# Kernel tuning notes

Hardware: AMD Instinct MI355X
Metric: run time of the kernel (lower is better)

Reference implementation:

```python
import jax, jax.numpy as jnp
import numpy as np
from jax import lax

B, L = 8, 2048
TOP_K = 30
NUM_RBF = 16
NUM_POS = 16
NODE_IN, EDGE_IN = 6, NUM_POS + NUM_RBF  # features_type='dist'
H = 128  # node_features == edge_features


def setup_inputs() -> dict:
    key = jax.random.key(0)
    ks = jax.random.split(key, 4)
    # coords scaled so pairwise distances span the RBF range [0, 20]
    X = jax.random.normal(ks[0], (B, L, 4, 3), dtype=jnp.float32) * 10.0
    mask = jnp.ones((B, L), dtype=jnp.float32)
    W_node = jax.random.normal(ks[1], (NODE_IN, H), dtype=jnp.float32) * 0.1
    b_node = jnp.zeros((H,), dtype=jnp.float32)
    W_edge = jax.random.normal(ks[2], (EDGE_IN, H), dtype=jnp.float32) * 0.1
    b_edge = jnp.zeros((H,), dtype=jnp.float32)
    gamma_n = jnp.ones((H,), dtype=jnp.float32)
    beta_n = jnp.zeros((H,), dtype=jnp.float32)
    gamma_e = jnp.ones((H,), dtype=jnp.float32)
    beta_e = jnp.zeros((H,), dtype=jnp.float32)
    return {"X": X, "mask": mask, "W_node": W_node, "b_node": b_node,
            "W_edge": W_edge, "b_edge": b_edge, "gamma_n": gamma_n,
            "beta_n": beta_n, "gamma_e": gamma_e, "beta_e": beta_e}


def _dist(X_ca, mask, eps=1e-6):
    # masked pairwise Euclidean distances + kNN (smallest)
    mask_2D = mask[:, None, :] * mask[:, :, None]            # [B,L,L]
    dX = X_ca[:, None, :, :] - X_ca[:, :, None, :]           # [B,L,L,3]
    D = mask_2D * jnp.sqrt(jnp.sum(dX * dX, axis=-1) + eps)  # [B,L,L]
    D_max = jnp.max(D, axis=-1, keepdims=True)
    D_adjust = D + (1.0 - mask_2D) * (D_max + 1.0)
    neg_D, E_idx = lax.top_k(-D_adjust, TOP_K)               # smallest-k
    return -neg_D, E_idx                                     # [B,L,K], [B,L,K]


def _rbf(D):
    D_mu = jnp.linspace(0.0, 20.0, NUM_RBF)                  # [R]
    D_sigma = 20.0 / NUM_RBF
    return jnp.exp(-(((D[..., None] - D_mu) / D_sigma) ** 2))  # [B,L,K,R]


def _positional_encodings(E_idx):
    # directional differential positional encodings
    N_nodes = E_idx.shape[1]
    ii = jnp.arange(N_nodes, dtype=jnp.float32)[None, :, None]
    d = (E_idx.astype(jnp.float32) - ii)[..., None]          # [B,L,K,1]
    freq = jnp.exp(jnp.arange(0, NUM_POS, 2, dtype=jnp.float32)
                   * (-(np.log(10000.0) / NUM_POS)))          # [P/2]
    angles = d * freq                                        # [B,L,K,P/2]
    return jnp.concatenate([jnp.cos(angles), jnp.sin(angles)], axis=-1)


def _dihedrals(X, eps=1e-7):
    # phi/psi/omega from N,CA,C backbone trace -> [B,L,6]
    b, n = X.shape[0], X.shape[1]
    Xb = X[:, :, :3, :].reshape(b, 3 * n, 3)
    dX = Xb[:, 1:, :] - Xb[:, :-1, :]
    U = dX / (jnp.linalg.norm(dX, axis=-1, keepdims=True) + 1e-8)
    u_2, u_1, u_0 = U[:, :-2], U[:, 1:-1], U[:, 2:]
    n_2 = jnp.cross(u_2, u_1)
    n_2 = n_2 / (jnp.linalg.norm(n_2, axis=-1, keepdims=True) + 1e-8)
    n_1 = jnp.cross(u_1, u_0)
    n_1 = n_1 / (jnp.linalg.norm(n_1, axis=-1, keepdims=True) + 1e-8)
    cosD = jnp.clip(jnp.sum(n_2 * n_1, axis=-1), -1.0 + eps, 1.0 - eps)
    Dang = jnp.sign(jnp.sum(u_2 * n_1, axis=-1)) * jnp.arccos(cosD)
    Dang = jnp.pad(Dang, ((0, 0), (1, 2)))
    Dang = Dang.reshape(b, n, 3)
    return jnp.concatenate([jnp.cos(Dang), jnp.sin(Dang)], axis=-1)


def _layer_norm(x, gamma, beta, eps=1e-5):
    mu = jnp.mean(x, axis=-1, keepdims=True)
    var = jnp.mean((x - mu) ** 2, axis=-1, keepdims=True)
    return (x - mu) * lax.rsqrt(var + eps) * gamma + beta


def reference(X, mask, W_node, b_node, W_edge, b_edge,
              gamma_n, beta_n, gamma_e, beta_e):
    X_ca = X[:, :, 1, :]
    D_neighbors, E_idx = _dist(X_ca, mask)
    E_positional = _positional_encodings(E_idx)              # [B,L,K,P]
    RBF = _rbf(D_neighbors)                                  # [B,L,K,R]
    V = _dihedrals(X)                                        # [B,L,6]
    E = jnp.concatenate([E_positional, RBF], axis=-1)        # [B,L,K,P+R]
    V = _layer_norm(V @ W_node + b_node, gamma_n, beta_n)
    E = _layer_norm(E @ W_edge + b_edge, gamma_e, beta_e)
    return V, E, E_idx
```

## Files before the change

### kernel.cpp

```cpp
#include <hip/hip_runtime.h>
#include <cstdint>
#include <cstddef>

#define NB 8
#define NL 2048
#define TOPK 30
#define NH 128
#define CAND_CAP 256

typedef unsigned long long ull;
typedef __attribute__((ext_vector_type(8))) short short8v;
typedef __attribute__((ext_vector_type(4))) float f32x4;

__device__ __forceinline__ short f2bf(float f) {
    unsigned int b = __float_as_uint(f);
    b += 0x7fffu + ((b >> 16) & 1u);
    return (short)(b >> 16);
}

__global__ __launch_bounds__(256) void vnx_kernel(
    const float* __restrict__ X, const float* __restrict__ mask,
    const float* __restrict__ Wn, const float* __restrict__ bn,
    const float* __restrict__ gn, const float* __restrict__ btn,
    float* __restrict__ V, float4* __restrict__ P)
{
    __shared__ float fsh[64][8];

    const int tid = threadIdx.x;
    const int node_base = blockIdx.x * 64;

    if (tid < 64) {
        const int ln   = tid;
        const int node = node_base + ln;
        const int b = node >> 11, i = node & (NL - 1);

        const int h0 = ln, h1 = ln + 64;
        float w0[6], w1[6];
        #pragma unroll
        for (int j = 0; j < 6; ++j) { w0[j] = Wn[j * NH + h0]; w1[j] = Wn[j * NH + h1]; }
        const float bb0 = bn[h0], bb1 = bn[h1];

        float st[35];
        {
            int idx = 0;
            #pragma unroll
            for (int j = 0; j < 6; ++j)
                #pragma unroll
                for (int k = j; k < 6; ++k)
                    st[idx++] = w0[j] * w0[k] + w1[j] * w1[k];
            #pragma unroll
            for (int j = 0; j < 6; ++j) st[21 + j] = w0[j] * bb0 + w1[j] * bb1;
            #pragma unroll
            for (int j = 0; j < 6; ++j) st[27 + j] = w0[j] + w1[j];
            st[33] = bb0 + bb1;
            st[34] = bb0 * bb0 + bb1 * bb1;
            #pragma unroll
            for (int q = 0; q < 35; ++q) {
                float vv = st[q];
                #pragma unroll
                for (int off = 32; off; off >>= 1) vv += __shfl_xor(vv, off);
                st[q] = vv;
            }
        }

        const float* XB = X + (size_t)b * NL * 12;
        const int rm1 = (i >= 1) ? i - 1 : 0;
        const int rp1 = (i <= NL - 2) ? i + 1 : NL - 1;
        float p[6][3];
        {
            const int rows[6]  = { rm1, i, i, i, rp1, rp1 };
            const int atoms[6] = { 2,   0, 1, 2, 0,   1   };
            #pragma unroll
            for (int k = 0; k < 6; ++k) {
                const float* q = XB + ((size_t)rows[k] * 4 + atoms[k]) * 3;
                p[k][0] = q[0]; p[k][1] = q[1]; p[k][2] = q[2];
            }
        }
        P[node] = make_float4(p[2][0], p[2][1], p[2][2], mask[node]);

        float uv[5][3], nv[4][3];
        #pragma unroll
        for (int k = 0; k < 5; ++k) {
            float vx = p[k+1][0] - p[k][0];
            float vy = p[k+1][1] - p[k][1];
            float vz = p[k+1][2] - p[k][2];
            float n = sqrtf(vx*vx + vy*vy + vz*vz) + 1e-8f;
            uv[k][0] = vx / n; uv[k][1] = vy / n; uv[k][2] = vz / n;
        }
        #pragma unroll
        for (int k = 0; k < 4; ++k) {
            float cx = uv[k][1]*uv[k+1][2] - uv[k][2]*uv[k+1][1];
            float cy = uv[k][2]*uv[k+1][0] - uv[k][0]*uv[k+1][2];
            float cz = uv[k][0]*uv[k+1][1] - uv[k][1]*uv[k+1][0];
            float n = sqrtf(cx*cx + cy*cy + cz*cz) + 1e-8f;
            nv[k][0] = cx / n; nv[k][1] = cy / n; nv[k][2] = cz / n;
        }
        float f[6];
        #pragma unroll
        for (int a = 0; a < 3; ++a) {
            bool valid = (a == 0) ? (i >= 1) : (i <= NL - 2);
            float cosD = nv[a][0]*nv[a+1][0] + nv[a][1]*nv[a+1][1] + nv[a][2]*nv[a+1][2];
            cosD = fminf(fmaxf(cosD, -1.0f + 1e-7f), 1.0f - 1e-7f);
            float sg = uv[a][0]*nv[a+1][0] + uv[a][1]*nv[a+1][1] + uv[a][2]*nv[a+1][2];
            float sgn = (sg > 0.0f) ? 1.0f : ((sg < 0.0f) ? -1.0f : 0.0f);
            float an = valid ? (sgn * acosf(cosD)) : 0.0f;
            f[a]     = cosf(an);
            f[3 + a] = sinf(an);
        }

        float s1 = st[33];
        #pragma unroll
        for (int j = 0; j < 6; ++j) s1 = fmaf(f[j], st[27 + j], s1);
        float qd = st[34];
        #pragma unroll
        for (int j = 0; j < 6; ++j) qd = fmaf(2.0f * f[j], st[21 + j], qd);
        {
            int idx = 0;
            #pragma unroll
            for (int j = 0; j < 6; ++j)
                #pragma unroll
                for (int k = j; k < 6; ++k) {
                    float coef = (j == k) ? 1.0f : 2.0f;
                    qd = fmaf(coef * f[j] * f[k], st[idx], qd);
                    ++idx;
                }
        }
        const float mean = s1 * (1.0f / 128.0f);
        const float var  = fmaxf(qd * (1.0f / 128.0f) - mean * mean, 0.0f);
        const float inv  = rsqrtf(var + 1e-5f);

        #pragma unroll
        for (int j = 0; j < 6; ++j) fsh[ln][j] = f[j];
        fsh[ln][6] = mean;
        fsh[ln][7] = inv;
    }
    __syncthreads();

    const int m  = tid & 31;
    const int ng = tid >> 5;
    const int h4 = m * 4;
    f32x4 w4[6];
    #pragma unroll
    for (int j = 0; j < 6; ++j) w4[j] = *(const f32x4*)&Wn[j * NH + h4];
    const f32x4 b4  = *(const f32x4*)&bn [h4];
    const f32x4 g4  = *(const f32x4*)&gn [h4];
    const f32x4 bt4 = *(const f32x4*)&btn[h4];

    #pragma unroll
    for (int it = 0; it < 8; ++it) {
        const int nn = it * 8 + ng;
        const float* fr = fsh[nn];
        f32x4 a = b4;
        #pragma unroll
        for (int j = 0; j < 6; ++j) {
            const float fj = fr[j];
            #pragma unroll
            for (int x = 0; x < 4; ++x) a[x] = fmaf(fj, w4[j][x], a[x]);
        }
        const float mn = fr[6], iv = fr[7];
        f32x4 o;
        #pragma unroll
        for (int x = 0; x < 4; ++x) o[x] = (a[x] - mn) * iv * g4[x] + bt4[x];
        *(f32x4*)&V[(size_t)(node_base + nn) * NH + h4] = o;
    }
}

__global__ __launch_bounds__(256) void topk_kernel(
    const float4* __restrict__ P,
    float* __restrict__ eidx, float* __restrict__ dnb)
{
    __shared__ float4 Ps[NL];
    __shared__ ull cand[4][CAND_CAP];

    const int tid = threadIdx.x;
    const int wv  = tid >> 6;
    const int ln  = tid & 63;
    const int row = blockIdx.x * 4 + wv;
    const int b   = row >> 11;
    const int i   = row & (NL - 1);

    const float4* Pb = P + (size_t)b * NL;
    #pragma unroll
    for (int q = 0; q < 8; ++q) Ps[tid + 256 * q] = Pb[tid + 256 * q];
    __syncthreads();

    const float4 pi = Ps[i];
    const float xi = pi.x, yi = pi.y, zi = pi.z, mi = pi.w;

    unsigned int u[32];
    float lm0 = 0.0f, lm1 = 0.0f, lm2 = 0.0f, lm3 = 0.0f;
    #pragma unroll
    for (int t = 0; t < 32; t += 4) {
        #pragma unroll
        for (int q = 0; q < 4; ++q) {
            const float4 pj = Ps[ln + 64 * (t + q)];
            float dx = xi - pj.x;
            float dy = yi - pj.y;
            float dz = zi - pj.z;
            float s = __fadd_rn(__fmul_rn(dx, dx), __fmul_rn(dy, dy));
            s = __fadd_rn(s, __fmul_rn(dz, dz));
            s = __fadd_rn(s, 1e-6f);
            float m2 = __fmul_rn(pj.w, mi);
            float d  = __fmul_rn(m2, __fsqrt_rn(s));
            u[t + q] = __float_as_uint(d) | ((m2 == 0.0f) ? 0x80000000u : 0u);
            if      (q == 0) lm0 = fmaxf(lm0, d);
            else if (q == 1) lm1 = fmaxf(lm1, d);
            else if (q == 2) lm2 = fmaxf(lm2, d);
            else             lm3 = fmaxf(lm3, d);
        }
    }
    float lmax = fmaxf(fmaxf(lm0, lm1), fmaxf(lm2, lm3));
    #pragma unroll
    for (int off = 32; off; off >>= 1) lmax = fmaxf(lmax, __shfl_xor(lmax, off));
    const unsigned int DMB = __float_as_uint(__fadd_rn(lmax, 1.0f));

    unsigned int um0 = 0xFFFFFFFFu, um1 = 0xFFFFFFFFu,
                 um2 = 0xFFFFFFFFu, um3 = 0xFFFFFFFFu;
    #pragma unroll
    for (int t = 0; t < 32; t += 4) {
        unsigned int b0 = (u[t+0] & 0x80000000u) ? DMB : u[t+0];
        unsigned int b1 = (u[t+1] & 0x80000000u) ? DMB : u[t+1];
        unsigned int b2 = (u[t+2] & 0x80000000u) ? DMB : u[t+2];
        unsigned int b3 = (u[t+3] & 0x80000000u) ? DMB : u[t+3];
        u[t+0] = b0; u[t+1] = b1; u[t+2] = b2; u[t+3] = b3;
        um0 = min(um0, b0); um1 = min(um1, b1);
        um2 = min(um2, b2); um3 = min(um3, b3);
    }
    unsigned int umin = min(min(um0, um1), min(um2, um3));

    unsigned int v = umin;
    #pragma unroll
    for (int k = 2; k <= 64; k <<= 1) {
        #pragma unroll
        for (int j = k >> 1; j > 0; j >>= 1) {
            unsigned int o = __shfl_xor(v, j);
            bool asc   = ((ln & k) == 0);
            bool lower = ((ln & j) == 0);
            v = (lower == asc) ? min(v, o) : max(v, o);
        }
    }
    const unsigned int T = __shfl(v, TOPK - 1);

    unsigned int base = 0;
    #pragma unroll
    for (int t = 0; t < 32; ++t) {
        bool act = u[t] <= T;
        ull m = __ballot(act);
        if (act) {
            unsigned int pos = base + (unsigned)__popcll(m & ((1ull << ln) - 1ull));
            if (pos < CAND_CAP)
                cand[wv][pos] = ((ull)u[t] << 32) | (unsigned)(ln + 64 * t);
        }
        base += (unsigned)__popcll(m);
    }
    const unsigned int cnt = base;

    float* eo  = eidx + (size_t)row * TOPK;
    float* dno = dnb  + (size_t)row * TOPK;

    if (cnt <= CAND_CAP) {
        ull k0 = ((unsigned)ln        < cnt) ? cand[wv][ln]        : ~0ULL;
        ull k1 = ((unsigned)ln +  64u < cnt) ? cand[wv][ln +  64]  : ~0ULL;
        ull k2 = ((unsigned)ln + 128u < cnt) ? cand[wv][ln + 128]  : ~0ULL;
        ull k3 = ((unsigned)ln + 192u < cnt) ? cand[wv][ln + 192]  : ~0ULL;
        int r0 = 0, r1 = 0, r2 = 0, r3 = 0;
        for (unsigned int p = 0; p < cnt; p += 4) {
            ull c0 = cand[wv][p];
            ull c1 = (p + 1 < cnt) ? cand[wv][p + 1] : ~0ULL;
            ull c2 = (p + 2 < cnt) ? cand[wv][p + 2] : ~0ULL;
            ull c3 = (p + 3 < cnt) ? cand[wv][p + 3] : ~0ULL;
            r0 += (c0 < k0) + (c1 < k0) + (c2 < k0) + (c3 < k0);
            r1 += (c0 < k1) + (c1 < k1) + (c2 < k1) + (c3 < k1);
            r2 += (c0 < k2) + (c1 < k2) + (c2 < k2) + (c3 < k2);
            r3 += (c0 < k3) + (c1 < k3) + (c2 < k3) + (c3 < k3);
        }
        if (r0 < TOPK) { eo[r0] = (float)(unsigned)(k0 & 0xFFFFFFFFu); dno[r0] = __uint_as_float((unsigned)(k0 >> 32)); }
        if (r1 < TOPK) { eo[r1] = (float)(unsigned)(k1 & 0xFFFFFFFFu); dno[r1] = __uint_as_float((unsigned)(k1 >> 32)); }
        if (r2 < TOPK) { eo[r2] = (float)(unsigned)(k2 & 0xFFFFFFFFu); dno[r2] = __uint_as_float((unsigned)(k2 >> 32)); }
        if (r3 < TOPK) { eo[r3] = (float)(unsigned)(k3 & 0xFFFFFFFFu); dno[r3] = __uint_as_float((unsigned)(k3 >> 32)); }
    } else {
        ull last = 0ULL;
        for (int k = 0; k < TOPK; ++k) {
            ull best = ~0ULL;
            #pragma unroll
            for (int t = 0; t < 32; ++t) {
                ull key = ((ull)u[t] << 32) | (unsigned)(ln + 64 * t);
                if (key > last && key < best) best = key;
            }
            #pragma unroll
            for (int off = 32; off; off >>= 1) {
                ull o = __shfl_xor(best, off);
                if (o < best) best = o;
            }
            if (ln == 0) {
                eo[k]  = (float)(unsigned)(best & 0xFFFFFFFFu);
                dno[k] = __uint_as_float((unsigned)(best >> 32));
            }
            last = best;
        }
    }
}

__global__ __launch_bounds__(256) void edge_kernel(
    const float* __restrict__ eidx, const float* __restrict__ dnb,
    const float* __restrict__ We, const float* __restrict__ be,
    const float* __restrict__ ge, const float* __restrict__ bte,
    float* __restrict__ E)
{
    __shared__ float ebuf[4][16][132];
    const int lane = threadIdx.x & 63;
    const int wv   = threadIdx.x >> 6;
    const int c    = lane & 15;
    const int g    = lane >> 4;
    const int wid  = (int)((blockIdx.x * blockDim.x + threadIdx.x) >> 6);
    const int nw   = (int)((gridDim.x * blockDim.x) >> 6);

    short8v W[8];
    #pragma unroll
    for (int t = 0; t < 8; ++t)
        #pragma unroll
        for (int e = 0; e < 8; ++e)
            W[t][e] = f2bf(We[(g * 8 + e) * NH + t * 16 + c]);

    float fcs[8];
    #pragma unroll
    for (int e = 0; e < 8; ++e) {
        if (g < 2) fcs[e] = expf((float)(2 * e) * -0.57564627f);
        else       fcs[e] = (float)((g - 2) * 8 + e) * (20.0f / 15.0f);
    }

    const int ntiles = NB * NL * TOPK / 16;
    for (int tile = wid; tile < ntiles; tile += nw) {
        const int e0   = tile * 16;
        const int edge = e0 + c;
        const float fidx = eidx[edge];
        const float Dv   = dnb[edge];
        const int   row  = edge / TOPK;
        const float d    = fidx - (float)(row & (NL - 1));

        short8v F;
        if (g == 0) {
            #pragma unroll
            for (int e = 0; e < 8; ++e) F[e] = f2bf(cosf(d * fcs[e]));
        } else if (g == 1) {
            #pragma unroll
            for (int e = 0; e < 8; ++e) F[e] = f2bf(sinf(d * fcs[e]));
        } else {
            #pragma unroll
            for (int e = 0; e < 8; ++e) {
                float tt = (Dv - fcs[e]) * 0.8f;
                F[e] = f2bf(expf(-tt * tt));
            }
        }

        f32x4 acc[8];
        const f32x4 zero = {0.0f, 0.0f, 0.0f, 0.0f};
        #pragma unroll
        for (int t = 0; t < 8; ++t)
            acc[t] = __builtin_amdgcn_mfma_f32_16x16x32_bf16(W[t], F, zero, 0, 0, 0);

        float s = 0.0f, s2 = 0.0f;
        #pragma unroll
        for (int t = 0; t < 8; ++t) {
            const f32x4 b4 = *(const f32x4*)&be[t * 16 + g * 4];
            #pragma unroll
            for (int j = 0; j < 4; ++j) {
                float vv = acc[t][j] + b4[j];
                acc[t][j] = vv;
                s  += vv;
                s2 = fmaf(vv, vv, s2);
            }
        }
        s  += __shfl_xor(s, 16);  s  += __shfl_xor(s, 32);
        s2 += __shfl_xor(s2, 16); s2 += __shfl_xor(s2, 32);
        const float mean = s * (1.0f / 128.0f);
        const float var  = fmaxf(s2 * (1.0f / 128.0f) - mean * mean, 0.0f);
        const float inv  = rsqrtf(var + 1e-5f);

        #pragma unroll
        for (int t = 0; t < 8; ++t) {
            const f32x4 g4  = *(const f32x4*)&ge [t * 16 + g * 4];
            const f32x4 bt4 = *(const f32x4*)&bte[t * 16 + g * 4];
            f32x4 o;
            #pragma unroll
            for (int j = 0; j < 4; ++j)
                o[j] = (acc[t][j] - mean) * inv * g4[j] + bt4[j];
            *(f32x4*)&ebuf[wv][c][t * 16 + g * 4] = o;
        }

        float* const Ebase = E + (size_t)e0 * NH;
        #pragma unroll
        for (int q = 0; q < 8; ++q) {
            const int fi = q * 256 + lane * 4;
            const int ce = fi >> 7;
            const int id = fi & 127;
            const f32x4 o = *(const f32x4*)&ebuf[wv][ce][id];
            __builtin_nontemporal_store(o, (f32x4*)&Ebase[(size_t)ce * NH + id]);
        }
    }
}

extern "C" void kernel_launch(void* const* d_in, const int* in_sizes, int n_in,
                              void* d_out, int out_size, void* d_ws, size_t ws_size,
                              hipStream_t stream)
{
    const float* X    = (const float*)d_in[0];
    const float* mask = (const float*)d_in[1];
    const float* Wn   = (const float*)d_in[2];
    const float* bn   = (const float*)d_in[3];
    const float* We   = (const float*)d_in[4];
    const float* be   = (const float*)d_in[5];
    const float* gn   = (const float*)d_in[6];
    const float* btn  = (const float*)d_in[7];
    const float* ge   = (const float*)d_in[8];
    const float* bte  = (const float*)d_in[9];

    float* out = (float*)d_out;
    float* V   = out;
    float* E   = V  + (size_t)NB * NL * NH;
    float* EI  = E  + (size_t)NB * NL * TOPK * NH;

    float4* P  = (float4*)d_ws;
    float* dnb = (float*)d_ws + 4 * (size_t)NB * NL;

    hipLaunchKernelGGL(vnx_kernel,  dim3(NB * NL / 64),  dim3(256), 0, stream,
                       X, mask, Wn, bn, gn, btn, V, P);
    hipLaunchKernelGGL(topk_kernel, dim3(NB * NL / 4),   dim3(256), 0, stream,
                       P, EI, dnb);
    hipLaunchKernelGGL(edge_kernel, dim3(1920),          dim3(256), 0, stream,
                       EI, dnb, We, be, ge, bte, E);
}
```

Measured before the change: 120.4 us.

## Merge node-feature kernel into edge kernel and load CA coords directly in topk

```diff
diff --git a/kernel.cpp b/kernel.cpp
--- a/kernel.cpp
+++ b/kernel.cpp
@@ -7,6 +7,8 @@
 #define TOPK 30
 #define NH 128
 #define CAND_CAP 256
+#define EDGE_BLOCKS 1920
+#define EDGE_WAVES (EDGE_BLOCKS * 4)
 
 typedef unsigned long long ull;
 typedef __attribute__((ext_vector_type(8))) short short8v;
@@ -18,170 +20,28 @@
     return (short)(b >> 16);
 }
 
-__global__ __launch_bounds__(256) void vnx_kernel(
+__global__ __launch_bounds__(512) void topk_kernel(
     const float* __restrict__ X, const float* __restrict__ mask,
-    const float* __restrict__ Wn, const float* __restrict__ bn,
-    const float* __restrict__ gn, const float* __restrict__ btn,
-    float* __restrict__ V, float4* __restrict__ P)
-{
-    __shared__ float fsh[64][8];
-
-    const int tid = threadIdx.x;
-    const int node_base = blockIdx.x * 64;
-
-    if (tid < 64) {
-        const int ln   = tid;
-        const int node = node_base + ln;
-        const int b = node >> 11, i = node & (NL - 1);
-
-        const int h0 = ln, h1 = ln + 64;
-        float w0[6], w1[6];
-        #pragma unroll
-        for (int j = 0; j < 6; ++j) { w0[j] = Wn[j * NH + h0]; w1[j] = Wn[j * NH + h1]; }
-        const float bb0 = bn[h0], bb1 = bn[h1];
-
-        float st[35];
-        {
-            int idx = 0;
-            #pragma unroll
-            for (int j = 0; j < 6; ++j)
-                #pragma unroll
-                for (int k = j; k < 6; ++k)
-                    st[idx++] = w0[j] * w0[k] + w1[j] * w1[k];
-            #pragma unroll
-            for (int j = 0; j < 6; ++j) st[21 + j] = w0[j] * bb0 + w1[j] * bb1;
-            #pragma unroll
-            for (int j = 0; j < 6; ++j) st[27 + j] = w0[j] + w1[j];
-            st[33] = bb0 + bb1;
-            st[34] = bb0 * bb0 + bb1 * bb1;
-            #pragma unroll
-            for (int q = 0; q < 35; ++q) {
-                float vv = st[q];
-                #pragma unroll
-                for (int off = 32; off; off >>= 1) vv += __shfl_xor(vv, off);
-                st[q] = vv;
-            }
-        }
-
-        const float* XB = X + (size_t)b * NL * 12;
-        const int rm1 = (i >= 1) ? i - 1 : 0;
-        const int rp1 = (i <= NL - 2) ? i + 1 : NL - 1;
-        float p[6][3];
-        {
-            const int rows[6]  = { rm1, i, i, i, rp1, rp1 };
-            const int atoms[6] = { 2,   0, 1, 2, 0,   1   };
-            #pragma unroll
-            for (int k = 0; k < 6; ++k) {
-                const float* q = XB + ((size_t)rows[k] * 4 + atoms[k]) * 3;
-                p[k][0] = q[0]; p[k][1] = q[1]; p[k][2] = q[2];
-            }
-        }
-        P[node] = make_float4(p[2][0], p[2][1], p[2][2], mask[node]);
-
-        float uv[5][3], nv[4][3];
-        #pragma unroll
-        for (int k = 0; k < 5; ++k) {
-            float vx = p[k+1][0] - p[k][0];
-            float vy = p[k+1][1] - p[k][1];
-            float vz = p[k+1][2] - p[k][2];
-            float n = sqrtf(vx*vx + vy*vy + vz*vz) + 1e-8f;
-            uv[k][0] = vx / n; uv[k][1] = vy / n; uv[k][2] = vz / n;
-        }
-        #pragma unroll
-        for (int k = 0; k < 4; ++k) {
-            float cx = uv[k][1]*uv[k+1][2] - uv[k][2]*uv[k+1][1];
-            float cy = uv[k][2]*uv[k+1][0] - uv[k][0]*uv[k+1][2];
-            float cz = uv[k][0]*uv[k+1][1] - uv[k][1]*uv[k+1][0];
-            float n = sqrtf(cx*cx + cy*cy + cz*cz) + 1e-8f;
-            nv[k][0] = cx / n; nv[k][1] = cy / n; nv[k][2] = cz / n;
-        }
-        float f[6];
-        #pragma unroll
-        for (int a = 0; a < 3; ++a) {
-            bool valid = (a == 0) ? (i >= 1) : (i <= NL - 2);
-            float cosD = nv[a][0]*nv[a+1][0] + nv[a][1]*nv[a+1][1] + nv[a][2]*nv[a+1][2];
-            cosD = fminf(fmaxf(cosD, -1.0f + 1e-7f), 1.0f - 1e-7f);
-            float sg = uv[a][0]*nv[a+1][0] + uv[a][1]*nv[a+1][1] + uv[a][2]*nv[a+1][2];
-            float sgn = (sg > 0.0f) ? 1.0f : ((sg < 0.0f) ? -1.0f : 0.0f);
-            float an = valid ? (sgn * acosf(cosD)) : 0.0f;
-            f[a]     = cosf(an);
-            f[3 + a] = sinf(an);
-        }
-
-        float s1 = st[33];
-        #pragma unroll
-        for (int j = 0; j < 6; ++j) s1 = fmaf(f[j], st[27 + j], s1);
-        float qd = st[34];
-        #pragma unroll
-        for (int j = 0; j < 6; ++j) qd = fmaf(2.0f * f[j], st[21 + j], qd);
-        {
-            int idx = 0;
-            #pragma unroll
-            for (int j = 0; j < 6; ++j)
-                #pragma unroll
-                for (int k = j; k < 6; ++k) {
-                    float coef = (j == k) ? 1.0f : 2.0f;
-                    qd = fmaf(coef * f[j] * f[k], st[idx], qd);
-                    ++idx;
-                }
-        }
-        const float mean = s1 * (1.0f / 128.0f);
-        const float var  = fmaxf(qd * (1.0f / 128.0f) - mean * mean, 0.0f);
-        const float inv  = rsqrtf(var + 1e-5f);
-
-        #pragma unroll
-        for (int j = 0; j < 6; ++j) fsh[ln][j] = f[j];
-        fsh[ln][6] = mean;
-        fsh[ln][7] = inv;
-    }
-    __syncthreads();
-
-    const int m  = tid & 31;
-    const int ng = tid >> 5;
-    const int h4 = m * 4;
-    f32x4 w4[6];
-    #pragma unroll
-    for (int j = 0; j < 6; ++j) w4[j] = *(const f32x4*)&Wn[j * NH + h4];
-    const f32x4 b4  = *(const f32x4*)&bn [h4];
-    const f32x4 g4  = *(const f32x4*)&gn [h4];
-    const f32x4 bt4 = *(const f32x4*)&btn[h4];
-
-    #pragma unroll
-    for (int it = 0; it < 8; ++it) {
-        const int nn = it * 8 + ng;
-        const float* fr = fsh[nn];
-        f32x4 a = b4;
-        #pragma unroll
-        for (int j = 0; j < 6; ++j) {
-            const float fj = fr[j];
-            #pragma unroll
-            for (int x = 0; x < 4; ++x) a[x] = fmaf(fj, w4[j][x], a[x]);
-        }
-        const float mn = fr[6], iv = fr[7];
-        f32x4 o;
-        #pragma unroll
-        for (int x = 0; x < 4; ++x) o[x] = (a[x] - mn) * iv * g4[x] + bt4[x];
-        *(f32x4*)&V[(size_t)(node_base + nn) * NH + h4] = o;
-    }
-}
-
-__global__ __launch_bounds__(256) void topk_kernel(
-    const float4* __restrict__ P,
     float* __restrict__ eidx, float* __restrict__ dnb)
 {
     __shared__ float4 Ps[NL];
-    __shared__ ull cand[4][CAND_CAP];
+    __shared__ ull cand[8][CAND_CAP];
 
     const int tid = threadIdx.x;
     const int wv  = tid >> 6;
     const int ln  = tid & 63;
-    const int row = blockIdx.x * 4 + wv;
+    const int row = blockIdx.x * 8 + wv;
     const int b   = row >> 11;
     const int i   = row & (NL - 1);
 
-    const float4* Pb = P + (size_t)b * NL;
-    #pragma unroll
-    for (int q = 0; q < 8; ++q) Ps[tid + 256 * q] = Pb[tid + 256 * q];
+    const float* Xb = X + (size_t)b * NL * 12;
+    const float* Mb = mask + (size_t)b * NL;
+    #pragma unroll
+    for (int q = 0; q < 4; ++q) {
+        const int j = tid + 512 * q;
+        const float* x = Xb + (size_t)j * 12 + 3;
+        Ps[j] = make_float4(x[0], x[1], x[2], Mb[j]);
+    }
     __syncthreads();
 
     const float4 pi = Ps[i];
@@ -301,102 +161,247 @@
     }
 }
 
-__global__ __launch_bounds__(256) void edge_kernel(
+__global__ __launch_bounds__(256) void edge_vn_kernel(
     const float* __restrict__ eidx, const float* __restrict__ dnb,
     const float* __restrict__ We, const float* __restrict__ be,
     const float* __restrict__ ge, const float* __restrict__ bte,
-    float* __restrict__ E)
+    float* __restrict__ E,
+    const float* __restrict__ X,  const float* __restrict__ Wn,
+    const float* __restrict__ bn, const float* __restrict__ gn,
+    const float* __restrict__ btn, float* __restrict__ V)
 {
-    __shared__ float ebuf[4][16][132];
-    const int lane = threadIdx.x & 63;
-    const int wv   = threadIdx.x >> 6;
-    const int c    = lane & 15;
-    const int g    = lane >> 4;
-    const int wid  = (int)((blockIdx.x * blockDim.x + threadIdx.x) >> 6);
-    const int nw   = (int)((gridDim.x * blockDim.x) >> 6);
-
-    short8v W[8];
-    #pragma unroll
-    for (int t = 0; t < 8; ++t)
-        #pragma unroll
-        for (int e = 0; e < 8; ++e)
-            W[t][e] = f2bf(We[(g * 8 + e) * NH + t * 16 + c]);
-
-    float fcs[8];
-    #pragma unroll
-    for (int e = 0; e < 8; ++e) {
-        if (g < 2) fcs[e] = expf((float)(2 * e) * -0.57564627f);
-        else       fcs[e] = (float)((g - 2) * 8 + e) * (20.0f / 15.0f);
-    }
-
-    const int ntiles = NB * NL * TOPK / 16;
-    for (int tile = wid; tile < ntiles; tile += nw) {
-        const int e0   = tile * 16;
-        const int edge = e0 + c;
-        const float fidx = eidx[edge];
-        const float Dv   = dnb[edge];
-        const int   row  = edge / TOPK;
-        const float d    = fidx - (float)(row & (NL - 1));
-
-        short8v F;
-        if (g == 0) {
-            #pragma unroll
-            for (int e = 0; e < 8; ++e) F[e] = f2bf(cosf(d * fcs[e]));
-        } else if (g == 1) {
-            #pragma unroll
-            for (int e = 0; e < 8; ++e) F[e] = f2bf(sinf(d * fcs[e]));
-        } else {
-            #pragma unroll
-            for (int e = 0; e < 8; ++e) {
-                float tt = (Dv - fcs[e]) * 0.8f;
-                F[e] = f2bf(expf(-tt * tt));
-            }
-        }
-
-        f32x4 acc[8];
-        const f32x4 zero = {0.0f, 0.0f, 0.0f, 0.0f};
+    __shared__ float shmem[4 * 16 * 132];
+
+    const int tid  = threadIdx.x;
+    const int lane = tid & 63;
+    const int wv   = tid >> 6;
+
+    if (blockIdx.x < EDGE_BLOCKS) {
+        float (*ebuf)[132] = (float(*)[132])(shmem + wv * 16 * 132);
+        const int c = lane & 15;
+        const int g = lane >> 4;
+        const int wid = blockIdx.x * 4 + wv;
+
+        short8v W[8];
         #pragma unroll
         for (int t = 0; t < 8; ++t)
-            acc[t] = __builtin_amdgcn_mfma_f32_16x16x32_bf16(W[t], F, zero, 0, 0, 0);
-
-        float s = 0.0f, s2 = 0.0f;
-        #pragma unroll
-        for (int t = 0; t < 8; ++t) {
-            const f32x4 b4 = *(const f32x4*)&be[t * 16 + g * 4];
-            #pragma unroll
-            for (int j = 0; j < 4; ++j) {
-                float vv = acc[t][j] + b4[j];
-                acc[t][j] = vv;
-                s  += vv;
-                s2 = fmaf(vv, vv, s2);
-            }
-        }
-        s  += __shfl_xor(s, 16);  s  += __shfl_xor(s, 32);
-        s2 += __shfl_xor(s2, 16); s2 += __shfl_xor(s2, 32);
-        const float mean = s * (1.0f / 128.0f);
-        const float var  = fmaxf(s2 * (1.0f / 128.0f) - mean * mean, 0.0f);
+            #pragma unroll
+            for (int e = 0; e < 8; ++e)
+                W[t][e] = f2bf(We[(g * 8 + e) * NH + t * 16 + c]);
+
+        float fcs[8];
+        #pragma unroll
+        for (int e = 0; e < 8; ++e) {
+            if (g < 2) fcs[e] = expf((float)(2 * e) * -0.57564627f);
+            else       fcs[e] = (float)((g - 2) * 8 + e) * (20.0f / 15.0f);
+        }
+
+        const int ntiles = NB * NL * TOPK / 16;
+        for (int tile = wid; tile < ntiles; tile += EDGE_WAVES) {
+            const int e0   = tile * 16;
+            const int edge = e0 + c;
+            const float fidx = eidx[edge];
+            const float Dv   = dnb[edge];
+            const int   row  = edge / TOPK;
+            const float d    = fidx - (float)(row & (NL - 1));
+
+            short8v F;
+            if (g == 0) {
+                #pragma unroll
+                for (int e = 0; e < 8; ++e) F[e] = f2bf(cosf(d * fcs[e]));
+            } else if (g == 1) {
+                #pragma unroll
+                for (int e = 0; e < 8; ++e) F[e] = f2bf(sinf(d * fcs[e]));
+            } else {
+                #pragma unroll
+                for (int e = 0; e < 8; ++e) {
+                    float tt = (Dv - fcs[e]) * 0.8f;
+                    F[e] = f2bf(expf(-tt * tt));
+                }
+            }
+
+            f32x4 acc[8];
+            const f32x4 zero = {0.0f, 0.0f, 0.0f, 0.0f};
+            #pragma unroll
+            for (int t = 0; t < 8; ++t)
+                acc[t] = __builtin_amdgcn_mfma_f32_16x16x32_bf16(W[t], F, zero, 0, 0, 0);
+
+            float s = 0.0f, s2 = 0.0f;
+            #pragma unroll
+            for (int t = 0; t < 8; ++t) {
+                const f32x4 b4 = *(const f32x4*)&be[t * 16 + g * 4];
+                #pragma unroll
+                for (int j = 0; j < 4; ++j) {
+                    float vv = acc[t][j] + b4[j];
+                    acc[t][j] = vv;
+                    s  += vv;
+                    s2 = fmaf(vv, vv, s2);
+                }
+            }
+            s  += __shfl_xor(s, 16);  s  += __shfl_xor(s, 32);
+            s2 += __shfl_xor(s2, 16); s2 += __shfl_xor(s2, 32);
+            const float mean = s * (1.0f / 128.0f);
+            const float var  = fmaxf(s2 * (1.0f / 128.0f) - mean * mean, 0.0f);
+            const float inv  = rsqrtf(var + 1e-5f);
+
+            #pragma unroll
+            for (int t = 0; t < 8; ++t) {
+                const f32x4 g4  = *(const f32x4*)&ge [t * 16 + g * 4];
+                const f32x4 bt4 = *(const f32x4*)&bte[t * 16 + g * 4];
+                f32x4 o;
+                #pragma unroll
+                for (int j = 0; j < 4; ++j)
+                    o[j] = (acc[t][j] - mean) * inv * g4[j] + bt4[j];
+                *(f32x4*)&ebuf[c][t * 16 + g * 4] = o;
+            }
+
+            float* const Ebase = E + (size_t)e0 * NH;
+            #pragma unroll
+            for (int q = 0; q < 8; ++q) {
+                const int fi = q * 256 + lane * 4;
+                const int ce = fi >> 7;
+                const int id = fi & 127;
+                const f32x4 o = *(const f32x4*)&ebuf[ce][id];
+                __builtin_nontemporal_store(o, (f32x4*)&Ebase[(size_t)ce * NH + id]);
+            }
+        }
+        return;
+    }
+
+    float (*fsh)[8] = (float(*)[8])shmem;
+    const int node_base = (blockIdx.x - EDGE_BLOCKS) * 64;
+
+    if (tid < 64) {
+        const int ln   = tid;
+        const int node = node_base + ln;
+        const int b = node >> 11, i = node & (NL - 1);
+
+        const int h0 = ln, h1 = ln + 64;
+        float w0[6], w1[6];
+        #pragma unroll
+        for (int j = 0; j < 6; ++j) { w0[j] = Wn[j * NH + h0]; w1[j] = Wn[j * NH + h1]; }
+        const float bb0 = bn[h0], bb1 = bn[h1];
+
+        float st[35];
+        {
+            int idx = 0;
+            #pragma unroll
+            for (int j = 0; j < 6; ++j)
+                #pragma unroll
+                for (int k = j; k < 6; ++k)
+                    st[idx++] = w0[j] * w0[k] + w1[j] * w1[k];
+            #pragma unroll
+            for (int j = 0; j < 6; ++j) st[21 + j] = w0[j] * bb0 + w1[j] * bb1;
+            #pragma unroll
+            for (int j = 0; j < 6; ++j) st[27 + j] = w0[j] + w1[j];
+            st[33] = bb0 + bb1;
+            st[34] = bb0 * bb0 + bb1 * bb1;
+            #pragma unroll
+            for (int q = 0; q < 35; ++q) {
+                float vv = st[q];
+                #pragma unroll
+                for (int off = 32; off; off >>= 1) vv += __shfl_xor(vv, off);
+                st[q] = vv;
+            }
+        }
+
+        const float* XB = X + (size_t)b * NL * 12;
+        const int rm1 = (i >= 1) ? i - 1 : 0;
+        const int rp1 = (i <= NL - 2) ? i + 1 : NL - 1;
+        float p[6][3];
+        {
+            const int rows[6]  = { rm1, i, i, i, rp1, rp1 };
+            const int atoms[6] = { 2,   0, 1, 2, 0,   1   };
+            #pragma unroll
+            for (int k = 0; k < 6; ++k) {
+                const float* q = XB + ((size_t)rows[k] * 4 + atoms[k]) * 3;
+                p[k][0] = q[0]; p[k][1] = q[1]; p[k][2] = q[2];
+            }
+        }
+        float uv[5][3], nv[4][3];
+        #pragma unroll
+        for (int k = 0; k < 5; ++k) {
+            float vx = p[k+1][0] - p[k][0];
+            float vy = p[k+1][1] - p[k][1];
+            float vz = p[k+1][2] - p[k][2];
+            float n = sqrtf(vx*vx + vy*vy + vz*vz) + 1e-8f;
+            uv[k][0] = vx / n; uv[k][1] = vy / n; uv[k][2] = vz / n;
+        }
+        #pragma unroll
+        for (int k = 0; k < 4; ++k) {
+            float cx = uv[k][1]*uv[k+1][2] - uv[k][2]*uv[k+1][1];
+            float cy = uv[k][2]*uv[k+1][0] - uv[k][0]*uv[k+1][2];
+            float cz = uv[k][0]*uv[k+1][1] - uv[k][1]*uv[k+1][0];
+            float n = sqrtf(cx*cx + cy*cy + cz*cz) + 1e-8f;
+            nv[k][0] = cx / n; nv[k][1] = cy / n; nv[k][2] = cz / n;
+        }
+        float f[6];
+        #pragma unroll
+        for (int a = 0; a < 3; ++a) {
+            bool valid = (a == 0) ? (i >= 1) : (i <= NL - 2);
+            float cosD = nv[a][0]*nv[a+1][0] + nv[a][1]*nv[a+1][1] + nv[a][2]*nv[a+1][2];
+            cosD = fminf(fmaxf(cosD, -1.0f + 1e-7f), 1.0f - 1e-7f);
+            float sg = uv[a][0]*nv[a+1][0] + uv[a][1]*nv[a+1][1] + uv[a][2]*nv[a+1][2];
+            float sgn = (sg > 0.0f) ? 1.0f : ((sg < 0.0f) ? -1.0f : 0.0f);
+            float an = valid ? (sgn * acosf(cosD)) : 0.0f;
+            f[a]     = cosf(an);
+            f[3 + a] = sinf(an);
+        }
+
+        float s1 = st[33];
+        #pragma unroll
+        for (int j = 0; j < 6; ++j) s1 = fmaf(f[j], st[27 + j], s1);
+        float qd = st[34];
+        #pragma unroll
+        for (int j = 0; j < 6; ++j) qd = fmaf(2.0f * f[j], st[21 + j], qd);
+        {
+            int idx = 0;
+            #pragma unroll
+            for (int j = 0; j < 6; ++j)
+                #pragma unroll
+                for (int k = j; k < 6; ++k) {
+                    float coef = (j == k) ? 1.0f : 2.0f;
+                    qd = fmaf(coef * f[j] * f[k], st[idx], qd);
+                    ++idx;
+                }
+        }
+        const float mean = s1 * (1.0f / 128.0f);
+        const float var  = fmaxf(qd * (1.0f / 128.0f) - mean * mean, 0.0f);
         const float inv  = rsqrtf(var + 1e-5f);
 
         #pragma unroll
-        for (int t = 0; t < 8; ++t) {
-            const f32x4 g4  = *(const f32x4*)&ge [t * 16 + g * 4];
-            const f32x4 bt4 = *(const f32x4*)&bte[t * 16 + g * 4];
-            f32x4 o;
-            #pragma unroll
-            for (int j = 0; j < 4; ++j)
-                o[j] = (acc[t][j] - mean) * inv * g4[j] + bt4[j];
-            *(f32x4*)&ebuf[wv][c][t * 16 + g * 4] = o;
-        }
-
-        float* const Ebase = E + (size_t)e0 * NH;
-        #pragma unroll
-        for (int q = 0; q < 8; ++q) {
-            const int fi = q * 256 + lane * 4;
-            const int ce = fi >> 7;
-            const int id = fi & 127;
-            const f32x4 o = *(const f32x4*)&ebuf[wv][ce][id];
-            __builtin_nontemporal_store(o, (f32x4*)&Ebase[(size_t)ce * NH + id]);
-        }
+        for (int j = 0; j < 6; ++j) fsh[ln][j] = f[j];
+        fsh[ln][6] = mean;
+        fsh[ln][7] = inv;
+    }
+    __syncthreads();
+
+    const int m  = tid & 31;
+    const int ng = tid >> 5;
+    const int h4 = m * 4;
+    f32x4 w4[6];
+    #pragma unroll
+    for (int j = 0; j < 6; ++j) w4[j] = *(const f32x4*)&Wn[j * NH + h4];
+    const f32x4 b4  = *(const f32x4*)&bn [h4];
+    const f32x4 g4  = *(const f32x4*)&gn [h4];
+    const f32x4 bt4 = *(const f32x4*)&btn[h4];
+
+    #pragma unroll
+    for (int it = 0; it < 8; ++it) {
+        const int nn = it * 8 + ng;
+        const float* fr = fsh[nn];
+        f32x4 a = b4;
+        #pragma unroll
+        for (int j = 0; j < 6; ++j) {
+            const float fj = fr[j];
+            #pragma unroll
+            for (int x = 0; x < 4; ++x) a[x] = fmaf(fj, w4[j][x], a[x]);
+        }
+        const float mn = fr[6], iv = fr[7];
+        f32x4 o;
+        #pragma unroll
+        for (int x = 0; x < 4; ++x) o[x] = (a[x] - mn) * iv * g4[x] + bt4[x];
+        *(f32x4*)&V[(size_t)(node_base + nn) * NH + h4] = o;
     }
 }
 
@@ -420,13 +425,10 @@
     float* E   = V  + (size_t)NB * NL * NH;
     float* EI  = E  + (size_t)NB * NL * TOPK * NH;
 
-    float4* P  = (float4*)d_ws;
-    float* dnb = (float*)d_ws + 4 * (size_t)NB * NL;
-
-    hipLaunchKernelGGL(vnx_kernel,  dim3(NB * NL / 64),  dim3(256), 0, stream,
-                       X, mask, Wn, bn, gn, btn, V, P);
-    hipLaunchKernelGGL(topk_kernel, dim3(NB * NL / 4),   dim3(256), 0, stream,
-                       P, EI, dnb);
-    hipLaunchKernelGGL(edge_kernel, dim3(1920),          dim3(256), 0, stream,
-                       EI, dnb, We, be, ge, bte, E);
+    float* dnb = (float*)d_ws;
+
+    hipLaunchKernelGGL(topk_kernel,    dim3(NB * NL / 8),      dim3(512), 0, stream,
+                       X, mask, EI, dnb);
+    hipLaunchKernelGGL(edge_vn_kernel, dim3(EDGE_BLOCKS + 256), dim3(256), 0, stream,
+                       EI, dnb, We, be, ge, bte, E, X, Wn, bn, gn, btn, V);
 }
```

New measurement: 113.4 us. -5.8%, faster.
